# Optimization experiments

Measured on AMD Instinct MI355X. Metric: run time of the kernel, lower is better.

The kernel has to match this reference:

```python
import jax, jax.numpy as jnp
import numpy as np

N = 10000        # nodes
E = 160000       # edges
IN = 1024        # in_channels
OUT = 512        # out_channels
H = 2 * OUT      # hidden width of conv1
EPS = 1e-5
NEG_SLOPE = 0.1


def setup_inputs() -> dict:
    key = jax.random.key(0)
    ks = jax.random.split(key, 8)
    s_in = 1.0 / np.sqrt(IN)
    s_h = 1.0 / np.sqrt(H)
    return {
        "x": jax.random.normal(ks[0], (N, IN), jnp.float32),
        "edge_index": jax.random.randint(ks[1], (2, E), 0, N, dtype=jnp.int64),
        "W1": jax.random.normal(ks[2], (IN, H), jnp.float32) * s_in,
        "b1": jnp.zeros((H,), jnp.float32),
        "Wm": jax.random.normal(ks[3], (H, OUT), jnp.float32) * s_h,
        "bm": jnp.zeros((OUT,), jnp.float32),
        "Ws": jax.random.normal(ks[4], (H, OUT), jnp.float32) * s_h,
        "bs": jnp.zeros((OUT,), jnp.float32),
        "gn_weight": jnp.ones((IN,), jnp.float32),
        "gn_bias": jnp.zeros((IN,), jnp.float32),
        "gn_mean_scale": jnp.ones((IN,), jnp.float32),
    }


def reference(x, edge_index, W1, b1, Wm, bm, Ws, bs, gn_weight, gn_bias, gn_mean_scale):
    # --- GraphNorm (eval, single graph: stats over all nodes) ---
    mean = jnp.mean(x, axis=0)                       # [IN]
    xc = x - gn_mean_scale * mean                    # [N, IN]
    var = jnp.mean(xc * xc, axis=0)                  # [IN]
    x = xc * jax.lax.rsqrt(var + EPS) * gn_weight + gn_bias

    # --- GCN normalization: add self loops, symmetric degree norm ---
    loop = jnp.arange(N, dtype=edge_index.dtype)
    src = jnp.concatenate([edge_index[0], loop])     # [E+N]
    dst = jnp.concatenate([edge_index[1], loop])     # [E+N]
    deg = jax.ops.segment_sum(jnp.ones_like(dst, dtype=x.dtype), dst, num_segments=N)
    deg_inv_sqrt = jax.lax.rsqrt(deg)                # deg >= 1 due to self loops
    enorm = deg_inv_sqrt[src] * deg_inv_sqrt[dst]    # [E+N]

    def gcn_conv(h, W, b):
        h = h @ W                                                        # dense GEMM
        agg = jax.ops.segment_sum(h[src] * enorm[:, None], dst, num_segments=N)
        return agg + b

    h = jax.nn.leaky_relu(gcn_conv(x, W1, b1), NEG_SLOPE)                # [N, H]
    mu = gcn_conv(h, Wm, bm)                                             # [N, OUT]
    logstd = gcn_conv(h, Ws, bs)                                         # [N, OUT]
    z = mu  # eval-mode reparametrize returns mu
    return (z, mu, logstd)
```

## Files before the change

kernel.cpp:

```cpp
#include <hip/hip_runtime.h>
#include <hip/hip_bf16.h>
#include <stdint.h>

#define NNODES 10000
#define NEDGES 160000
#define INCH 1024
#define HCH 1024
#define OUTCH 512
#define MPAD 10112
#define EPSV 1e-5f
#define NEG 0.1f
#define NSB 625
#define NSB2 32

typedef unsigned short u16;
typedef __bf16 bf16x8 __attribute__((ext_vector_type(8)));
typedef float f32x4 __attribute__((ext_vector_type(4)));
typedef __attribute__((address_space(1))) unsigned int gu32;
typedef __attribute__((address_space(3))) unsigned int lu32;

#define GL16(g, l) __builtin_amdgcn_global_load_lds((const gu32*)(g), (lu32*)(l), 16, 0, 0)

__device__ __forceinline__ float bf2f(u16 u) {
    union { unsigned int i; float f; } v; v.i = ((unsigned int)u) << 16; return v.f;
}
__device__ __forceinline__ u16 f2bf(float f) {
    union { float f; unsigned int i; } v; v.f = f;
    unsigned int r = v.i + 0x7fffu + ((v.i >> 16) & 1u);
    return (u16)(r >> 16);
}

__global__ __launch_bounds__(256) void cast_stats_k(const float* __restrict__ x,
                                                    u16* __restrict__ xn,
                                                    float* __restrict__ psum,
                                                    float* __restrict__ psq) {
    int c = threadIdx.x * 4;
    int r0 = blockIdx.x * 16;
    float s0 = 0.f, s1 = 0.f, s2 = 0.f, s3 = 0.f;
    float q0 = 0.f, q1 = 0.f, q2 = 0.f, q3 = 0.f;
#pragma unroll
    for (int r = 0; r < 16; ++r) {
        size_t off = (size_t)(r0 + r) * INCH + c;
        float4 v = *(const float4*)(x + off);
        ushort4 o;
        o.x = f2bf(v.x); o.y = f2bf(v.y); o.z = f2bf(v.z); o.w = f2bf(v.w);
        *(ushort4*)(xn + off) = o;
        float f0 = bf2f(o.x), f1 = bf2f(o.y), f2 = bf2f(o.z), f3 = bf2f(o.w);
        s0 += f0; s1 += f1; s2 += f2; s3 += f3;
        q0 += f0 * f0; q1 += f1 * f1; q2 += f2 * f2; q3 += f3 * f3;
    }
    size_t pb = (size_t)blockIdx.x * 1024 + c;
    *(float4*)(psum + pb) = make_float4(s0, s1, s2, s3);
    *(float4*)(psq + pb)  = make_float4(q0, q1, q2, q3);
}

__global__ __launch_bounds__(256) void reduce1_k(const float* __restrict__ psum,
                                                 const float* __restrict__ psq,
                                                 float* __restrict__ psum2,
                                                 float* __restrict__ psq2) {
    int c = threadIdx.x * 4;
    int b0 = blockIdx.x * 20;
    int b1 = min(b0 + 20, NSB);
    f32x4 s = {0.f, 0.f, 0.f, 0.f}, q = {0.f, 0.f, 0.f, 0.f};
    for (int b = b0; b < b1; ++b) {
        f32x4 vs = *(const f32x4*)(psum + (size_t)b * 1024 + c);
        f32x4 vq = *(const f32x4*)(psq + (size_t)b * 1024 + c);
        s += vs; q += vq;
    }
    *(f32x4*)(psum2 + (size_t)blockIdx.x * 1024 + c) = s;
    *(f32x4*)(psq2 + (size_t)blockIdx.x * 1024 + c) = q;
}

__global__ __launch_bounds__(256) void scale2_k(const float* __restrict__ psum2,
                                                const float* __restrict__ psq2,
                                                const float* __restrict__ gms,
                                                const float* __restrict__ gw,
                                                const float* __restrict__ gb,
                                                float* __restrict__ sc, float* __restrict__ sh) {
    int c = blockIdx.x * 256 + threadIdx.x;
    float s = 0.f, q = 0.f;
#pragma unroll
    for (int b = 0; b < NSB2; ++b) {
        s += psum2[(size_t)b * 1024 + c];
        q += psq2[(size_t)b * 1024 + c];
    }
    const float invn = 1.0f / NNODES;
    float m = s * invn;
    float msq = q * invn;
    float g = gms[c];
    float var = msq - g * (2.0f - g) * m * m;
    float scale = rsqrtf(var + EPSV) * gw[c];
    sc[c] = scale;
    sh[c] = gb[c] - g * m * scale;
}

__global__ void c1_k(const float* __restrict__ W1, const float* __restrict__ sh,
                     float* __restrict__ c1) {
    int j = blockIdx.x * 256 + threadIdx.x;
    int k0 = blockIdx.y * 128;
    float a = 0.f;
#pragma unroll 4
    for (int k = k0; k < k0 + 128; ++k) a += sh[k] * W1[(size_t)k * HCH + j];
    atomicAdd(&c1[j], a);
}

__global__ __launch_bounds__(256) void wt1_k(const float* __restrict__ W,
                                             const float* __restrict__ sc,
                                             u16* __restrict__ Bt) {
    __shared__ u16 t[64][68];
    int k0 = blockIdx.y * 64, c0 = blockIdx.x * 64;
    int tc = (threadIdx.x & 15) * 4;
    int tk = threadIdx.x >> 4;
#pragma unroll
    for (int i = 0; i < 64; i += 16) {
        float scr = sc[k0 + tk + i];
        float4 v = *(const float4*)(W + (size_t)(k0 + tk + i) * HCH + c0 + tc);
        t[tc + 0][tk + i] = f2bf(v.x * scr);
        t[tc + 1][tk + i] = f2bf(v.y * scr);
        t[tc + 2][tk + i] = f2bf(v.z * scr);
        t[tc + 3][tk + i] = f2bf(v.w * scr);
    }
    __syncthreads();
    int wk = (threadIdx.x & 15) * 4;
    int wc = threadIdx.x >> 4;
#pragma unroll
    for (int i = 0; i < 64; i += 16) {
        ushort4 o;
        o.x = t[wc + i][wk + 0]; o.y = t[wc + i][wk + 1];
        o.z = t[wc + i][wk + 2]; o.w = t[wc + i][wk + 3];
        *(ushort4*)(Bt + (size_t)(c0 + wc + i) * 1024 + k0 + wk) = o;
    }
}

__global__ __launch_bounds__(256) void wt2_k(const float* __restrict__ Wm,
                                             const float* __restrict__ Ws,
                                             u16* __restrict__ Bt) {
    __shared__ u16 t[64][68];
    int k0 = blockIdx.y * 64, c0 = blockIdx.x * 64;
    const float* W = (c0 < OUTCH) ? Wm : Ws;
    int cb = (c0 < OUTCH) ? c0 : c0 - OUTCH;
    int tc = (threadIdx.x & 15) * 4;
    int tk = threadIdx.x >> 4;
#pragma unroll
    for (int i = 0; i < 64; i += 16) {
        float4 v = *(const float4*)(W + (size_t)(k0 + tk + i) * OUTCH + cb + tc);
        t[tc + 0][tk + i] = f2bf(v.x);
        t[tc + 1][tk + i] = f2bf(v.y);
        t[tc + 2][tk + i] = f2bf(v.z);
        t[tc + 3][tk + i] = f2bf(v.w);
    }
    __syncthreads();
    int wk = (threadIdx.x & 15) * 4;
    int wc = threadIdx.x >> 4;
#pragma unroll
    for (int i = 0; i < 64; i += 16) {
        ushort4 o;
        o.x = t[wc + i][wk + 0]; o.y = t[wc + i][wk + 1];
        o.z = t[wc + i][wk + 2]; o.w = t[wc + i][wk + 3];
        *(ushort4*)(Bt + (size_t)(c0 + wc + i) * 1024 + k0 + wk) = o;
    }
}

__global__ void deg_k(const int* __restrict__ dst, int* __restrict__ cnt) {
    int e = blockIdx.x * 256 + threadIdx.x;
    if (e < NEDGES) atomicAdd(&cnt[dst[e]], 1);
}
__global__ void dis_k(const int* __restrict__ cnt, float* __restrict__ dis,
                      float* __restrict__ rowsum) {
    int i = blockIdx.x * 256 + threadIdx.x;
    if (i < NNODES) {
        float d = rsqrtf((float)(cnt[i] + 1));
        dis[i] = d;
        rowsum[i] = d * d;
    }
}
__global__ void scan_k(const int* __restrict__ cnt, int* __restrict__ row_ptr,
                       int* __restrict__ cursor) {
    __shared__ int sm[256];
    int tid = threadIdx.x;
    const int per = 40;
    int base = tid * per;
    int s = 0;
    for (int i = 0; i < per; ++i) { int idx = base + i; if (idx < NNODES) s += cnt[idx]; }
    sm[tid] = s; __syncthreads();
    for (int off = 1; off < 256; off <<= 1) {
        int v = (tid >= off) ? sm[tid - off] : 0;
        __syncthreads();
        sm[tid] += v;
        __syncthreads();
    }
    int run = (tid == 0) ? 0 : sm[tid - 1];
    for (int i = 0; i < per; ++i) {
        int idx = base + i;
        if (idx < NNODES) { row_ptr[idx] = run; cursor[idx] = run; run += cnt[idx]; }
    }
    if (tid == 255) row_ptr[NNODES] = sm[255];
}
__global__ void fill_k(const int* __restrict__ src, const int* __restrict__ dst,
                       const float* __restrict__ dis, int* __restrict__ cursor,
                       int2* __restrict__ csr, float* __restrict__ rowsum) {
    int e = blockIdx.x * 256 + threadIdx.x;
    if (e >= NEDGES) return;
    int s = src[e], d = dst[e];
    float w = dis[s] * dis[d];
    int pos = atomicAdd(&cursor[d], 1);
    csr[pos] = make_int2(s, __float_as_int(w));
    atomicAdd(&rowsum[d], w);
}

template<int MODE>
__global__ __launch_bounds__(256) void aggs_k(const u16* __restrict__ in, u16* __restrict__ out,
                      const int* __restrict__ row_ptr, const int2* __restrict__ csr,
                      const float* __restrict__ dis,
                      const float* __restrict__ bias, const float* __restrict__ rowsum,
                      const float* __restrict__ c1) {
    int slice = blockIdx.x;
    int node = blockIdx.y * 4 + (threadIdx.x >> 6);
    int lane = threadIdx.x & 63;
    int ch = slice * 128 + lane * 2;
    float dv = dis[node];
    float selfw = dv * dv;
    unsigned int sv = *(const unsigned int*)(in + (size_t)node * HCH + ch);
    float a0 = bf2f((u16)(sv & 0xffff)) * selfw;
    float a1 = bf2f((u16)(sv >> 16)) * selfw;
    float b0 = 0.f, b1v = 0.f, c0 = 0.f, c1v = 0.f, d0 = 0.f, d1 = 0.f, e0a = 0.f, e1a = 0.f;
    int e0 = row_ptr[node], e1 = row_ptr[node + 1];
    int e = e0;
    for (; e + 4 <= e1; e += 4) {
        int2 sw0 = csr[e + 0];
        int2 sw1 = csr[e + 1];
        int2 sw2 = csr[e + 2];
        int2 sw3 = csr[e + 3];
        unsigned int v0 = *(const unsigned int*)(in + (size_t)sw0.x * HCH + ch);
        unsigned int v1 = *(const unsigned int*)(in + (size_t)sw1.x * HCH + ch);
        unsigned int v2 = *(const unsigned int*)(in + (size_t)sw2.x * HCH + ch);
        unsigned int v3 = *(const unsigned int*)(in + (size_t)sw3.x * HCH + ch);
        float w0 = __int_as_float(sw0.y), w1 = __int_as_float(sw1.y);
        float w2 = __int_as_float(sw2.y), w3 = __int_as_float(sw3.y);
        a0 += bf2f((u16)(v0 & 0xffff)) * w0; a1 += bf2f((u16)(v0 >> 16)) * w0;
        b0 += bf2f((u16)(v1 & 0xffff)) * w1; b1v += bf2f((u16)(v1 >> 16)) * w1;
        c0 += bf2f((u16)(v2 & 0xffff)) * w2; c1v += bf2f((u16)(v2 >> 16)) * w2;
        d0 += bf2f((u16)(v3 & 0xffff)) * w3; d1 += bf2f((u16)(v3 >> 16)) * w3;
    }
    for (; e < e1; ++e) {
        int2 sw = csr[e];
        float w = __int_as_float(sw.y);
        unsigned int v = *(const unsigned int*)(in + (size_t)sw.x * HCH + ch);
        e0a += bf2f((u16)(v & 0xffff)) * w; e1a += bf2f((u16)(v >> 16)) * w;
    }
    float r0 = ((a0 + b0) + (c0 + d0)) + e0a;
    float r1 = ((a1 + b1v) + (c1v + d1)) + e1a;
    if (MODE == 1) {
        float rs = rowsum[node];
        float2 bb = *(const float2*)(bias + ch);
        float2 cc = *(const float2*)(c1 + ch);
        r0 += rs * cc.x + bb.x;
        r1 += rs * cc.y + bb.y;
        r0 = r0 > 0.f ? r0 : NEG * r0;
        r1 = r1 > 0.f ? r1 : NEG * r1;
    }
    unsigned int o = (unsigned int)f2bf(r0) | ((unsigned int)f2bf(r1) << 16);
    *(unsigned int*)(out + (size_t)node * HCH + ch) = o;
}

template<int EPI>
__global__ __launch_bounds__(256) void gemm_k(
    const u16* __restrict__ A, const u16* __restrict__ Bt,
    u16* __restrict__ Cbf, float* __restrict__ out,
    const float* __restrict__ bm, const float* __restrict__ bs) {
    __shared__ u16 As[128 * 32];
    __shared__ u16 Bs[128 * 32];
    const int orig = blockIdx.x;
    const int wg = (orig & 7) * 79 + (orig >> 3);
    const int row0 = (wg >> 3) * 128;
    const int col0 = (wg & 7) * 128;
    const int tid = threadIdx.x;
    const int wave = tid >> 6;
    const int lane = tid & 63;
    const int wr = wave >> 1, wc = wave & 1;
    const int sr = lane >> 2;
    const int sc = (lane & 3) * 8;
    u16* AsW0 = &As[(wave * 16) * 32];
    u16* AsW1 = &As[(64 + wave * 16) * 32];
    u16* BsW0 = &Bs[(wave * 16) * 32];
    u16* BsW1 = &Bs[(64 + wave * 16) * 32];
    const u16* Ag0 = A + (size_t)(row0 + wave * 16 + sr) * 1024 + sc;
    const u16* Ag1 = A + (size_t)(row0 + 64 + wave * 16 + sr) * 1024 + sc;
    const u16* Bg0 = Bt + (size_t)(col0 + wave * 16 + sr) * 1024 + sc;
    const u16* Bg1 = Bt + (size_t)(col0 + 64 + wave * 16 + sr) * 1024 + sc;

    f32x4 acc[4][4] = {};
    const int arow = lane & 15;
    const int ak = (lane >> 4) * 8;
    for (int kk = 0; kk < 1024; kk += 32) {
        GL16(Ag0 + kk, AsW0);
        GL16(Ag1 + kk, AsW1);
        GL16(Bg0 + kk, BsW0);
        GL16(Bg1 + kk, BsW1);
        __syncthreads();
        bf16x8 af[4], bf[4];
#pragma unroll
        for (int m = 0; m < 4; ++m)
            af[m] = *reinterpret_cast<const bf16x8*>(&As[(wr * 64 + m * 16 + arow) * 32 + ak]);
#pragma unroll
        for (int n = 0; n < 4; ++n)
            bf[n] = *reinterpret_cast<const bf16x8*>(&Bs[(wc * 64 + n * 16 + arow) * 32 + ak]);
#pragma unroll
        for (int m = 0; m < 4; ++m)
#pragma unroll
            for (int n = 0; n < 4; ++n)
                acc[m][n] = __builtin_amdgcn_mfma_f32_16x16x32_bf16(af[m], bf[n], acc[m][n], 0, 0, 0);
        __syncthreads();
    }
    const int crow = (lane >> 4) * 4;
    const int ccol = lane & 15;
    if (EPI == 0) {
#pragma unroll
        for (int m = 0; m < 4; ++m) {
            int rbase = row0 + wr * 64 + m * 16 + crow;
#pragma unroll
            for (int n = 0; n < 4; ++n) {
                int col = col0 + wc * 64 + n * 16 + ccol;
                f32x4 v = acc[m][n];
#pragma unroll
                for (int r = 0; r < 4; ++r)
                    Cbf[(size_t)(rbase + r) * 1024 + col] = f2bf(v[r]);
            }
        }
    } else {
        const size_t NOUT = (size_t)NNODES * OUTCH;
#pragma unroll
        for (int n = 0; n < 4; ++n) {
            int col = col0 + wc * 64 + n * 16 + ccol;
            bool lo = col < OUTCH;
            int colo = lo ? col : col - OUTCH;
            float bias = lo ? bm[colo] : bs[colo];
#pragma unroll
            for (int m = 0; m < 4; ++m) {
                int rbase = row0 + wr * 64 + m * 16 + crow;
                f32x4 v = acc[m][n];
#pragma unroll
                for (int r = 0; r < 4; ++r) {
                    int rr = rbase + r;
                    if (rr < NNODES) {
                        float val = v[r] + bias;
                        if (lo) {
                            out[(size_t)rr * OUTCH + colo] = val;
                            out[NOUT + (size_t)rr * OUTCH + colo] = val;
                        } else {
                            out[2 * NOUT + (size_t)rr * OUTCH + colo] = val;
                        }
                    }
                }
            }
        }
    }
}

extern "C" void kernel_launch(void* const* d_in, const int* in_sizes, int n_in,
                              void* d_out, int out_size, void* d_ws, size_t ws_size,
                              hipStream_t stream) {
    const float* x   = (const float*)d_in[0];
    const int*   ei  = (const int*)d_in[1];
    const float* W1  = (const float*)d_in[2];
    const float* b1  = (const float*)d_in[3];
    const float* Wm  = (const float*)d_in[4];
    const float* bm  = (const float*)d_in[5];
    const float* Ws  = (const float*)d_in[6];
    const float* bs  = (const float*)d_in[7];
    const float* gw  = (const float*)d_in[8];
    const float* gb  = (const float*)d_in[9];
    const float* gms = (const float*)d_in[10];
    const int* srcI = ei;
    const int* dstI = ei + NEDGES;

    char* ws = (char*)d_ws;
    const size_t SBIG = (size_t)MPAD * 1024 * 2;
    u16* xn   = (u16*)(ws);
    u16* h1g  = (u16*)(ws + SBIG);
    u16* h    = (u16*)(ws + 2 * SBIG);
    u16* aggh = xn;
    u16* Bt1  = (u16*)(ws + 3 * SBIG);
    u16* Bt2  = (u16*)(ws + 3 * SBIG + (size_t)2 * 1024 * 1024);
    float* psum  = (float*)(ws + SBIG);
    float* psq   = (float*)(ws + SBIG + (size_t)NSB * 4096);
    float* psum2 = (float*)(ws + SBIG + (size_t)2 * NSB * 4096);
    float* psq2  = (float*)(ws + SBIG + (size_t)2 * NSB * 4096 + (size_t)NSB2 * 4096);
    char* small   = ws + 3 * SBIG + (size_t)4 * 1024 * 1024;
    int*   cnt    = (int*)(small);
    float* rowsum = (float*)(small + 40960);
    float* c1     = (float*)(small + 81920);
    int*   row_ptr= (int*)(small + 86016);
    int*   cursor = (int*)(small + 126976);
    float* dis    = (float*)(small + 167936);
    int2*  csr    = (int2*)(small + 208896);
    float* sc     = (float*)(small + 1488896);
    float* sh     = (float*)(small + 1492992);

    hipMemsetAsync(small, 0, 86016, stream);

    cast_stats_k<<<NSB, 256, 0, stream>>>(x, xn, psum, psq);
    deg_k<<<625, 256, 0, stream>>>(dstI, cnt);
    dis_k<<<40, 256, 0, stream>>>(cnt, dis, rowsum);
    scan_k<<<1, 256, 0, stream>>>(cnt, row_ptr, cursor);
    fill_k<<<625, 256, 0, stream>>>(srcI, dstI, dis, cursor, csr, rowsum);
    reduce1_k<<<NSB2, 256, 0, stream>>>(psum, psq, psum2, psq2);
    scale2_k<<<4, 256, 0, stream>>>(psum2, psq2, gms, gw, gb, sc, sh);
    wt1_k<<<dim3(16, 16), 256, 0, stream>>>(W1, sc, Bt1);
    c1_k<<<dim3(4, 8), 256, 0, stream>>>(W1, sh, c1);
    wt2_k<<<dim3(16, 16), 256, 0, stream>>>(Wm, Ws, Bt2);

    gemm_k<0><<<632, 256, 0, stream>>>(xn, Bt1, h1g, nullptr, nullptr, nullptr);
    aggs_k<1><<<dim3(8, 2500), 256, 0, stream>>>(h1g, h, row_ptr, csr, dis, b1, rowsum, c1);
    aggs_k<0><<<dim3(8, 2500), 256, 0, stream>>>(h, aggh, row_ptr, csr, dis, nullptr, nullptr, nullptr);
    gemm_k<1><<<632, 256, 0, stream>>>(aggh, Bt2, nullptr, (float*)d_out, bm, bs);
}
```

Measured before the change: 369.9 us.

## Swizzle GEMM LDS tiles, use 2D grid, fold dis_k into scan

The GEMM now stores each 16-byte k-group at a position XOR-swizzled by row, via the global-to-LDS load address, and reads it back with the matching swizzle. This is meant to cut LDS bank conflicts on the MFMA fragment reads. The 1D XCD-remapped block index is replaced by a plain 2D grid, which gives up the earlier L2 locality mapping. The deg-inverse-sqrt computation is folded into the single-block scan kernel, removing one launch, and some preprocessing launches are reordered.

```diff
diff --git a/kernel.cpp b/kernel.cpp
--- a/kernel.cpp
+++ b/kernel.cpp
@@ -165,17 +165,9 @@
     int e = blockIdx.x * 256 + threadIdx.x;
     if (e < NEDGES) atomicAdd(&cnt[dst[e]], 1);
 }
-__global__ void dis_k(const int* __restrict__ cnt, float* __restrict__ dis,
-                      float* __restrict__ rowsum) {
-    int i = blockIdx.x * 256 + threadIdx.x;
-    if (i < NNODES) {
-        float d = rsqrtf((float)(cnt[i] + 1));
-        dis[i] = d;
-        rowsum[i] = d * d;
-    }
-}
 __global__ void scan_k(const int* __restrict__ cnt, int* __restrict__ row_ptr,
-                       int* __restrict__ cursor) {
+                       int* __restrict__ cursor, float* __restrict__ dis,
+                       float* __restrict__ rowsum) {
     __shared__ int sm[256];
     int tid = threadIdx.x;
     const int per = 40;
@@ -192,7 +184,12 @@
     int run = (tid == 0) ? 0 : sm[tid - 1];
     for (int i = 0; i < per; ++i) {
         int idx = base + i;
-        if (idx < NNODES) { row_ptr[idx] = run; cursor[idx] = run; run += cnt[idx]; }
+        if (idx < NNODES) {
+            row_ptr[idx] = run; cursor[idx] = run; run += cnt[idx];
+            float d = rsqrtf((float)(cnt[idx] + 1));
+            dis[idx] = d;
+            rowsum[idx] = d * d;
+        }
     }
     if (tid == 255) row_ptr[NNODES] = sm[255];
 }
@@ -270,28 +267,26 @@
     const float* __restrict__ bm, const float* __restrict__ bs) {
     __shared__ u16 As[128 * 32];
     __shared__ u16 Bs[128 * 32];
-    const int orig = blockIdx.x;
-    const int wg = (orig & 7) * 79 + (orig >> 3);
-    const int row0 = (wg >> 3) * 128;
-    const int col0 = (wg & 7) * 128;
     const int tid = threadIdx.x;
     const int wave = tid >> 6;
     const int lane = tid & 63;
+    const int row0 = blockIdx.y * 128;
+    const int col0 = blockIdx.x * 128;
     const int wr = wave >> 1, wc = wave & 1;
     const int sr = lane >> 2;
-    const int sc = (lane & 3) * 8;
+    const int sgx = ((lane & 3) ^ ((sr >> 1) & 3)) * 8;
     u16* AsW0 = &As[(wave * 16) * 32];
     u16* AsW1 = &As[(64 + wave * 16) * 32];
     u16* BsW0 = &Bs[(wave * 16) * 32];
     u16* BsW1 = &Bs[(64 + wave * 16) * 32];
-    const u16* Ag0 = A + (size_t)(row0 + wave * 16 + sr) * 1024 + sc;
-    const u16* Ag1 = A + (size_t)(row0 + 64 + wave * 16 + sr) * 1024 + sc;
-    const u16* Bg0 = Bt + (size_t)(col0 + wave * 16 + sr) * 1024 + sc;
-    const u16* Bg1 = Bt + (size_t)(col0 + 64 + wave * 16 + sr) * 1024 + sc;
+    const u16* Ag0 = A + (size_t)(row0 + wave * 16 + sr) * 1024 + sgx;
+    const u16* Ag1 = A + (size_t)(row0 + 64 + wave * 16 + sr) * 1024 + sgx;
+    const u16* Bg0 = Bt + (size_t)(col0 + wave * 16 + sr) * 1024 + sgx;
+    const u16* Bg1 = Bt + (size_t)(col0 + 64 + wave * 16 + sr) * 1024 + sgx;
 
     f32x4 acc[4][4] = {};
     const int arow = lane & 15;
-    const int ak = (lane >> 4) * 8;
+    const int gsel = ((lane >> 4) ^ ((arow >> 1) & 3)) * 8;
     for (int kk = 0; kk < 1024; kk += 32) {
         GL16(Ag0 + kk, AsW0);
         GL16(Ag1 + kk, AsW1);
@@ -301,10 +296,10 @@
         bf16x8 af[4], bf[4];
 #pragma unroll
         for (int m = 0; m < 4; ++m)
-            af[m] = *reinterpret_cast<const bf16x8*>(&As[(wr * 64 + m * 16 + arow) * 32 + ak]);
+            af[m] = *reinterpret_cast<const bf16x8*>(&As[(wr * 64 + m * 16 + arow) * 32 + gsel]);
 #pragma unroll
         for (int n = 0; n < 4; ++n)
-            bf[n] = *reinterpret_cast<const bf16x8*>(&Bs[(wc * 64 + n * 16 + arow) * 32 + ak]);
+            bf[n] = *reinterpret_cast<const bf16x8*>(&Bs[(wc * 64 + n * 16 + arow) * 32 + gsel]);
 #pragma unroll
         for (int m = 0; m < 4; ++m)
 #pragma unroll
@@ -399,19 +394,18 @@
 
     hipMemsetAsync(small, 0, 86016, stream);
 
+    deg_k<<<625, 256, 0, stream>>>(dstI, cnt);
+    scan_k<<<1, 256, 0, stream>>>(cnt, row_ptr, cursor, dis, rowsum);
+    fill_k<<<625, 256, 0, stream>>>(srcI, dstI, dis, cursor, csr, rowsum);
+    wt2_k<<<dim3(16, 16), 256, 0, stream>>>(Wm, Ws, Bt2);
     cast_stats_k<<<NSB, 256, 0, stream>>>(x, xn, psum, psq);
-    deg_k<<<625, 256, 0, stream>>>(dstI, cnt);
-    dis_k<<<40, 256, 0, stream>>>(cnt, dis, rowsum);
-    scan_k<<<1, 256, 0, stream>>>(cnt, row_ptr, cursor);
-    fill_k<<<625, 256, 0, stream>>>(srcI, dstI, dis, cursor, csr, rowsum);
     reduce1_k<<<NSB2, 256, 0, stream>>>(psum, psq, psum2, psq2);
     scale2_k<<<4, 256, 0, stream>>>(psum2, psq2, gms, gw, gb, sc, sh);
     wt1_k<<<dim3(16, 16), 256, 0, stream>>>(W1, sc, Bt1);
     c1_k<<<dim3(4, 8), 256, 0, stream>>>(W1, sh, c1);
-    wt2_k<<<dim3(16, 16), 256, 0, stream>>>(Wm, Ws, Bt2);
-
-    gemm_k<0><<<632, 256, 0, stream>>>(xn, Bt1, h1g, nullptr, nullptr, nullptr);
+
+    gemm_k<0><<<dim3(8, 79), 256, 0, stream>>>(xn, Bt1, h1g, nullptr, nullptr, nullptr);
     aggs_k<1><<<dim3(8, 2500), 256, 0, stream>>>(h1g, h, row_ptr, csr, dis, b1, rowsum, c1);
     aggs_k<0><<<dim3(8, 2500), 256, 0, stream>>>(h, aggh, row_ptr, csr, dis, nullptr, nullptr, nullptr);
-    gemm_k<1><<<632, 256, 0, stream>>>(aggh, Bt2, nullptr, (float*)d_out, bm, bs);
-}
+    gemm_k<1><<<dim3(8, 79), 256, 0, stream>>>(aggh, Bt2, nullptr, (float*)d_out, bm, bs);
+}
```

After: 387.4 us. 4.7% more time.
